# Kernel optimization log

Measured on AMD Instinct MI355X. Metric: run time of the kernel, lower is better.

The kernel has to match this reference:

```python
import jax, jax.numpy as jnp
import numpy as np

B, H, S, D = 4, 16, 2048, 64


def setup_inputs() -> dict:
    key = jax.random.key(0)
    kq, kk, kv = jax.random.split(key, 3)
    q = jax.random.normal(kq, (B, H, S, D), dtype=jnp.float32)
    k = jax.random.normal(kk, (B, H, S, D), dtype=jnp.float32)
    v = jax.random.normal(kv, (B, H, S, D), dtype=jnp.float32)
    return {"q": q, "k": k, "v": v}


def reference(q, k, v):
    # scores: [B, H, S_q, S_k]
    scale = 1.0 / jnp.sqrt(jnp.asarray(q.shape[-1], q.dtype))
    scores = jnp.einsum("bhqd,bhkd->bhqk", q, k) * scale
    attn = jax.nn.softmax(scores, axis=-1)
    # dropout p=0.0 -> identity
    return jnp.einsum("bhqk,bhkd->bhqd", attn, v)
```

## Files before the change

kernel.cpp:

```cpp
#include <hip/hip_runtime.h>


#define S_LEN 2048
#define D_LEN 64
#define QT    128
#define TK    64
#define THREADS 256
#define KSTR  72

typedef __attribute__((ext_vector_type(8)))  short bf16x8;
typedef __attribute__((ext_vector_type(16))) float f32x16;

#if __has_builtin(__builtin_amdgcn_exp2f)
#define FAST_EXP2(x) __builtin_amdgcn_exp2f(x)
#else
#define FAST_EXP2(x) __expf((x) * 0.69314718055994531f)
#endif

__device__ __forceinline__ unsigned pk2(float a, float b) {
    unsigned r;
    asm("v_cvt_pk_bf16_f32 %0, %1, %2" : "=v"(r) : "v"(a), "v"(b));
    return r;
}

__global__ __launch_bounds__(THREADS, 4)
void attn_mfma32(const float* __restrict__ qg,
                 const float* __restrict__ kg,
                 const float* __restrict__ vg,
                 float* __restrict__ og)
{
    __shared__ alignas(16) unsigned short Ks[TK * KSTR];
    __shared__ alignas(16) unsigned short Vt[D_LEN * KSTR];
    __shared__ alignas(16) unsigned short Ps[4 * 32 * KSTR];

    const int tid  = threadIdx.x;
    const int w    = tid >> 6;
    const int lane = tid & 63;
    const int q31  = lane & 31;
    const int hi   = lane >> 5;

    const int bh    = blockIdx.x >> 4;
    const int qblk  = blockIdx.x & 15;
    const int qrow0 = qblk * QT + w * 32;

    const float* kbase = kg + (size_t)bh * S_LEN * D_LEN;
    const float* vbase = vg + (size_t)bh * S_LEN * D_LEN;

    const float c = 0.125f * 1.4426950408889634f;
    bf16x8 qf[4];
    {
        const float* qp = qg + ((size_t)bh * S_LEN + qrow0 + q31) * D_LEN + hi * 8;
#pragma unroll
        for (int kf = 0; kf < 4; ++kf) {
            float4 a = ((const float4*)(qp + kf * 16))[0];
            float4 b = ((const float4*)(qp + kf * 16))[1];
            uint4 u = make_uint4(pk2(a.x * c, a.y * c), pk2(a.z * c, a.w * c),
                                 pk2(b.x * c, b.y * c), pk2(b.z * c, b.w * c));
            qf[kf] = __builtin_bit_cast(bf16x8, u);
        }
    }

    f32x16 o0, o1;
#pragma unroll
    for (int i = 0; i < 16; ++i) { o0[i] = 0.f; o1[i] = 0.f; }
    float lsum = 0.f;

    const int skey = tid >> 2;
    const int sc   = tid & 3;
    const float4* kptr = (const float4*)kbase + (size_t)skey * 16 + sc * 4;
    const float* vptr = vbase + (size_t)(w * 16) * D_LEN + lane;

    float4 kreg[4];
    float  vreg[16];
#pragma unroll
    for (int i = 0; i < 4; ++i) kreg[i] = kptr[i];
#pragma unroll
    for (int r = 0; r < 16; ++r) vreg[r] = vptr[r * 64];

    unsigned short* pw = &Ps[w * 32 * KSTR];

    for (int t0 = 0; t0 < S_LEN; t0 += TK) {
        __syncthreads();
        {
            uint4 u0 = make_uint4(pk2(kreg[0].x, kreg[0].y), pk2(kreg[0].z, kreg[0].w),
                                  pk2(kreg[1].x, kreg[1].y), pk2(kreg[1].z, kreg[1].w));
            uint4 u1 = make_uint4(pk2(kreg[2].x, kreg[2].y), pk2(kreg[2].z, kreg[2].w),
                                  pk2(kreg[3].x, kreg[3].y), pk2(kreg[3].z, kreg[3].w));
            *(uint4*)&Ks[skey * KSTR + sc * 16]     = u0;
            *(uint4*)&Ks[skey * KSTR + sc * 16 + 8] = u1;
            uint4 v0 = make_uint4(pk2(vreg[0], vreg[1]),   pk2(vreg[2], vreg[3]),
                                  pk2(vreg[4], vreg[5]),   pk2(vreg[6], vreg[7]));
            uint4 v1 = make_uint4(pk2(vreg[8], vreg[9]),   pk2(vreg[10], vreg[11]),
                                  pk2(vreg[12], vreg[13]), pk2(vreg[14], vreg[15]));
            *(uint4*)&Vt[lane * KSTR + w * 16]     = v0;
            *(uint4*)&Vt[lane * KSTR + w * 16 + 8] = v1;
        }
        __syncthreads();

        if (t0 + TK < S_LEN) {
            const float4* kn = kptr + (size_t)(t0 + TK) * 16;
#pragma unroll
            for (int i = 0; i < 4; ++i) kreg[i] = kn[i];
            const float* vn = vptr + (size_t)(t0 + TK) * D_LEN;
#pragma unroll
            for (int r = 0; r < 16; ++r) vreg[r] = vn[r * 64];
        }

#pragma unroll
        for (int kt = 0; kt < 2; ++kt) {
            f32x16 s;
#pragma unroll
            for (int i = 0; i < 16; ++i) s[i] = 0.f;
#pragma unroll
            for (int kf = 0; kf < 4; ++kf) {
                bf16x8 ka = *(const bf16x8*)&Ks[(kt * 32 + q31) * KSTR + kf * 16 + hi * 8];
                s = __builtin_amdgcn_mfma_f32_32x32x16_bf16(ka, qf[kf], s, 0, 0, 0);
            }
#pragma unroll
            for (int g = 0; g < 4; ++g) {
                float p0 = FAST_EXP2(s[4 * g + 0]);
                float p1 = FAST_EXP2(s[4 * g + 1]);
                float p2 = FAST_EXP2(s[4 * g + 2]);
                float p3 = FAST_EXP2(s[4 * g + 3]);
                lsum += (p0 + p1) + (p2 + p3);
                uint2 u = { pk2(p0, p1), pk2(p2, p3) };
                *(uint2*)&pw[q31 * KSTR + kt * 32 + g * 8 + hi * 4] = u;
            }
        }
        __builtin_amdgcn_s_waitcnt(0xC07F);

#pragma unroll
        for (int kq = 0; kq < 4; ++kq) {
            bf16x8 pb  = *(const bf16x8*)&pw[q31 * KSTR + kq * 16 + hi * 8];
            bf16x8 va0 = *(const bf16x8*)&Vt[q31 * KSTR + kq * 16 + hi * 8];
            bf16x8 va1 = *(const bf16x8*)&Vt[(32 + q31) * KSTR + kq * 16 + hi * 8];
            o0 = __builtin_amdgcn_mfma_f32_32x32x16_bf16(va0, pb, o0, 0, 0, 0);
            o1 = __builtin_amdgcn_mfma_f32_32x32x16_bf16(va1, pb, o1, 0, 0, 0);
        }
    }

    float l = lsum + __shfl_xor(lsum, 32);
    const float inv = 1.0f / l;
    float* ob = og + ((size_t)bh * S_LEN + qrow0 + q31) * D_LEN;
#pragma unroll
    for (int g = 0; g < 4; ++g) {
        float4 f0 = make_float4(o0[4 * g + 0] * inv, o0[4 * g + 1] * inv,
                                o0[4 * g + 2] * inv, o0[4 * g + 3] * inv);
        ((float4*)(ob + g * 8 + hi * 4))[0] = f0;
        float4 f1 = make_float4(o1[4 * g + 0] * inv, o1[4 * g + 1] * inv,
                                o1[4 * g + 2] * inv, o1[4 * g + 3] * inv);
        ((float4*)(ob + 32 + g * 8 + hi * 4))[0] = f1;
    }
}

extern "C" void kernel_launch(void* const* d_in, const int* in_sizes, int n_in,
                              void* d_out, int out_size, void* d_ws, size_t ws_size,
                              hipStream_t stream)
{
    const float* q = (const float*)d_in[0];
    const float* k = (const float*)d_in[1];
    const float* v = (const float*)d_in[2];
    float* out = (float*)d_out;

    dim3 grid(64 * (S_LEN / QT));
    dim3 block(THREADS);
    attn_mfma32<<<grid, block, 0, stream>>>(q, k, v, out);
}
```

Baseline: 215.3 us.

## Double-buffer K/V tiles, keep P in registers via permlane swap, swizzle blocks

K and V tiles now alternate between two LDS buffers, so each iteration needs one barrier instead of two and the next tile is staged after compute. The P matrix no longer goes through LDS: the bf16-packed probabilities are rearranged into the MFMA B-operand layout with v_permlane32_swap and fed straight to the PV MFMA. Block indices are also swizzled so neighbouring workgroups handle different heads. LDS per block grows for the double buffers, and correctness depends on the permlane layout matching the MFMA operand layout.

```diff
diff --git a/kernel.cpp b/kernel.cpp
--- a/kernel.cpp
+++ b/kernel.cpp
@@ -7,6 +7,7 @@
 #define TK    64
 #define THREADS 256
 #define KSTR  72
+#define NT    (S_LEN / TK)
 
 typedef __attribute__((ext_vector_type(8)))  short bf16x8;
 typedef __attribute__((ext_vector_type(16))) float f32x16;
@@ -23,15 +24,18 @@
     return r;
 }
 
+__device__ __forceinline__ void pl32(unsigned& a, unsigned& b) {
+    asm("v_permlane32_swap_b32 %0, %1" : "+v"(a), "+v"(b));
+}
+
 __global__ __launch_bounds__(THREADS, 4)
 void attn_mfma32(const float* __restrict__ qg,
                  const float* __restrict__ kg,
                  const float* __restrict__ vg,
                  float* __restrict__ og)
 {
-    __shared__ alignas(16) unsigned short Ks[TK * KSTR];
-    __shared__ alignas(16) unsigned short Vt[D_LEN * KSTR];
-    __shared__ alignas(16) unsigned short Ps[4 * 32 * KSTR];
+    __shared__ alignas(16) unsigned short Ks[2][TK * KSTR];
+    __shared__ alignas(16) unsigned short Vt[2][D_LEN * KSTR];
 
     const int tid  = threadIdx.x;
     const int w    = tid >> 6;
@@ -39,8 +43,9 @@
     const int q31  = lane & 31;
     const int hi   = lane >> 5;
 
-    const int bh    = blockIdx.x >> 4;
-    const int qblk  = blockIdx.x & 15;
+    const int swz   = (blockIdx.x & 7) * 128 + (blockIdx.x >> 3);
+    const int bh    = swz >> 4;
+    const int qblk  = swz & 15;
     const int qrow0 = qblk * QT + w * 32;
 
     const float* kbase = kg + (size_t)bh * S_LEN * D_LEN;
@@ -77,31 +82,32 @@
 #pragma unroll
     for (int r = 0; r < 16; ++r) vreg[r] = vptr[r * 64];
 
-    unsigned short* pw = &Ps[w * 32 * KSTR];
+    auto stage = [&](int buf) {
+        uint4 u0 = make_uint4(pk2(kreg[0].x, kreg[0].y), pk2(kreg[0].z, kreg[0].w),
+                              pk2(kreg[1].x, kreg[1].y), pk2(kreg[1].z, kreg[1].w));
+        uint4 u1 = make_uint4(pk2(kreg[2].x, kreg[2].y), pk2(kreg[2].z, kreg[2].w),
+                              pk2(kreg[3].x, kreg[3].y), pk2(kreg[3].z, kreg[3].w));
+        *(uint4*)&Ks[buf][skey * KSTR + sc * 16]     = u0;
+        *(uint4*)&Ks[buf][skey * KSTR + sc * 16 + 8] = u1;
+        uint4 v0 = make_uint4(pk2(vreg[0], vreg[1]),   pk2(vreg[2], vreg[3]),
+                              pk2(vreg[4], vreg[5]),   pk2(vreg[6], vreg[7]));
+        uint4 v1 = make_uint4(pk2(vreg[8], vreg[9]),   pk2(vreg[10], vreg[11]),
+                              pk2(vreg[12], vreg[13]), pk2(vreg[14], vreg[15]));
+        *(uint4*)&Vt[buf][lane * KSTR + w * 16]     = v0;
+        *(uint4*)&Vt[buf][lane * KSTR + w * 16 + 8] = v1;
+    };
 
-    for (int t0 = 0; t0 < S_LEN; t0 += TK) {
-        __syncthreads();
-        {
-            uint4 u0 = make_uint4(pk2(kreg[0].x, kreg[0].y), pk2(kreg[0].z, kreg[0].w),
-                                  pk2(kreg[1].x, kreg[1].y), pk2(kreg[1].z, kreg[1].w));
-            uint4 u1 = make_uint4(pk2(kreg[2].x, kreg[2].y), pk2(kreg[2].z, kreg[2].w),
-                                  pk2(kreg[3].x, kreg[3].y), pk2(kreg[3].z, kreg[3].w));
-            *(uint4*)&Ks[skey * KSTR + sc * 16]     = u0;
-            *(uint4*)&Ks[skey * KSTR + sc * 16 + 8] = u1;
-            uint4 v0 = make_uint4(pk2(vreg[0], vreg[1]),   pk2(vreg[2], vreg[3]),
-                                  pk2(vreg[4], vreg[5]),   pk2(vreg[6], vreg[7]));
-            uint4 v1 = make_uint4(pk2(vreg[8], vreg[9]),   pk2(vreg[10], vreg[11]),
-                                  pk2(vreg[12], vreg[13]), pk2(vreg[14], vreg[15]));
-            *(uint4*)&Vt[lane * KSTR + w * 16]     = v0;
-            *(uint4*)&Vt[lane * KSTR + w * 16 + 8] = v1;
-        }
-        __syncthreads();
+    stage(0);
+    __syncthreads();
 
-        if (t0 + TK < S_LEN) {
-            const float4* kn = kptr + (size_t)(t0 + TK) * 16;
+    for (int t = 0; t < NT; ++t) {
+        const int cur = t & 1;
+
+        if (t + 1 < NT) {
+            const float4* kn = kptr + (size_t)(t + 1) * (TK * 16);
 #pragma unroll
             for (int i = 0; i < 4; ++i) kreg[i] = kn[i];
-            const float* vn = vptr + (size_t)(t0 + TK) * D_LEN;
+            const float* vn = vptr + (size_t)(t + 1) * (TK * D_LEN);
 #pragma unroll
             for (int r = 0; r < 16; ++r) vreg[r] = vn[r * 64];
         }
@@ -113,29 +119,34 @@
             for (int i = 0; i < 16; ++i) s[i] = 0.f;
 #pragma unroll
             for (int kf = 0; kf < 4; ++kf) {
-                bf16x8 ka = *(const bf16x8*)&Ks[(kt * 32 + q31) * KSTR + kf * 16 + hi * 8];
+                bf16x8 ka = *(const bf16x8*)&Ks[cur][(kt * 32 + q31) * KSTR + kf * 16 + hi * 8];
                 s = __builtin_amdgcn_mfma_f32_32x32x16_bf16(ka, qf[kf], s, 0, 0, 0);
             }
 #pragma unroll
-            for (int g = 0; g < 4; ++g) {
-                float p0 = FAST_EXP2(s[4 * g + 0]);
-                float p1 = FAST_EXP2(s[4 * g + 1]);
-                float p2 = FAST_EXP2(s[4 * g + 2]);
-                float p3 = FAST_EXP2(s[4 * g + 3]);
-                lsum += (p0 + p1) + (p2 + p3);
-                uint2 u = { pk2(p0, p1), pk2(p2, p3) };
-                *(uint2*)&pw[q31 * KSTR + kt * 32 + g * 8 + hi * 4] = u;
+            for (int f = 0; f < 2; ++f) {
+                const int b = f * 8;
+                float p0 = FAST_EXP2(s[b + 0]), p1 = FAST_EXP2(s[b + 1]);
+                float p2 = FAST_EXP2(s[b + 2]), p3 = FAST_EXP2(s[b + 3]);
+                float p4 = FAST_EXP2(s[b + 4]), p5 = FAST_EXP2(s[b + 5]);
+                float p6 = FAST_EXP2(s[b + 6]), p7 = FAST_EXP2(s[b + 7]);
+                lsum += ((p0 + p1) + (p2 + p3)) + ((p4 + p5) + (p6 + p7));
+                unsigned a0 = pk2(p0, p1), a1 = pk2(p4, p5);
+                unsigned b0 = pk2(p2, p3), b1 = pk2(p6, p7);
+                pl32(a0, a1);
+                pl32(b0, b1);
+                uint4 u = make_uint4(a0, b0, a1, b1);
+                bf16x8 pb = __builtin_bit_cast(bf16x8, u);
+                const int kq = kt * 2 + f;
+                bf16x8 va0 = *(const bf16x8*)&Vt[cur][q31 * KSTR + kq * 16 + hi * 8];
+                bf16x8 va1 = *(const bf16x8*)&Vt[cur][(32 + q31) * KSTR + kq * 16 + hi * 8];
+                o0 = __builtin_amdgcn_mfma_f32_32x32x16_bf16(va0, pb, o0, 0, 0, 0);
+                o1 = __builtin_amdgcn_mfma_f32_32x32x16_bf16(va1, pb, o1, 0, 0, 0);
             }
         }
-        __builtin_amdgcn_s_waitcnt(0xC07F);
 
-#pragma unroll
-        for (int kq = 0; kq < 4; ++kq) {
-            bf16x8 pb  = *(const bf16x8*)&pw[q31 * KSTR + kq * 16 + hi * 8];
-            bf16x8 va0 = *(const bf16x8*)&Vt[q31 * KSTR + kq * 16 + hi * 8];
-            bf16x8 va1 = *(const bf16x8*)&Vt[(32 + q31) * KSTR + kq * 16 + hi * 8];
-            o0 = __builtin_amdgcn_mfma_f32_32x32x16_bf16(va0, pb, o0, 0, 0, 0);
-            o1 = __builtin_amdgcn_mfma_f32_32x32x16_bf16(va1, pb, o1, 0, 0, 0);
+        if (t + 1 < NT) {
+            stage(cur ^ 1);
+            __syncthreads();
         }
     }
 
```

Result: faster. 209.8 us (-2.6%).
